# Performance work log

Hardware: AMD Instinct MI355X
Metric: run time of the kernel (lower is better)

## Reference

```python
import jax, jax.numpy as jnp
import numpy as np
import math

B = 2048
NOSC = 64            # oscillators per modality
M = 3                # modalities (audio, text, vision) in sorted order
BDIM = 256           # binding_dim
DT = 0.01
NSTEPS = 10
DIMS = [512, 768, 1024]  # audio, text, vision
TWO_PI = 2.0 * math.pi


def setup_inputs() -> dict:
    key = jax.random.key(0)
    ks = iter(jax.random.split(key, 40))
    d = {}
    names = ['a', 't', 'v']
    for name, dim, x_key in zip(names, DIMS, ['x_audio', 'x_text', 'x_vision']):
        d[x_key] = jax.random.normal(next(ks), (B, dim), dtype=jnp.float32)
        s = 1.0 / math.sqrt(dim)
        d[f'Wf_{name}'] = jax.random.uniform(next(ks), (BDIM, dim), jnp.float32, -s, s)
        d[f'bf_{name}'] = jax.random.uniform(next(ks), (BDIM,), jnp.float32, -s, s)
        d[f'Wp_{name}'] = jax.random.uniform(next(ks), (NOSC, dim), jnp.float32, -s, s)
        d[f'bp_{name}'] = jax.random.uniform(next(ks), (NOSC,), jnp.float32, -s, s)
    # omegas: randn*0.1 + 1.0 + i*0.5 for i-th sorted modality
    for i, name in enumerate(names):
        d[f'omega_{name}'] = jax.random.normal(next(ks), (NOSC,), jnp.float32) * 0.1 + 1.0 + i * 0.5
    N = M * NOSC
    d['inter_coupling'] = jax.random.normal(next(ks), (N, N), jnp.float32) * 0.1
    s = 1.0 / math.sqrt(BDIM * M)
    d['W_fusion'] = jax.random.uniform(next(ks), (BDIM, BDIM * M), jnp.float32, -s, s)
    d['b_fusion'] = jax.random.uniform(next(ks), (BDIM,), jnp.float32, -s, s)
    return d


def reference(x_audio, x_text, x_vision,
              Wf_a, bf_a, Wp_a, bp_a,
              Wf_t, bf_t, Wp_t, bp_t,
              Wf_v, bf_v, Wp_v, bp_v,
              omega_a, omega_t, omega_v,
              inter_coupling, W_fusion, b_fusion):
    def enc(x, Wf, bf, Wp, bp):
        encoded = x @ Wf.T + bf                       # (B, BDIM)
        phases = (x @ Wp.T + bp) % TWO_PI             # (B, NOSC)
        return encoded, phases

    e_a, p_a = enc(x_audio, Wf_a, bf_a, Wp_a, bp_a)
    e_t, p_t = enc(x_text, Wf_t, bf_t, Wp_t, bp_t)
    e_v, p_v = enc(x_vision, Wf_v, bf_v, Wp_v, bp_v)

    phases = jnp.concatenate([p_a, p_t, p_v], axis=-1)        # (B, N)
    omega = jnp.concatenate([omega_a, omega_t, omega_v])      # (N,)
    K = (inter_coupling + inter_coupling.T) * 0.5             # (N, N)
    N = phases.shape[-1]

    def step(ph, _):
        diff = ph[:, :, None] - ph[:, None, :]                # (B, N, N)
        forces = jnp.einsum('ij,bij->bi', K, jnp.sin(diff)) / N
        ph = (ph + DT * (omega[None, :] + forces)) % TWO_PI
        return ph, None

    phases, _ = jax.lax.scan(step, phases, None, length=NSTEPS)

    pm = [phases[:, i * NOSC:(i + 1) * NOSC] for i in range(M)]  # per-modality

    # PLV between banks a,b: |mean_{i,j} exp(i(a_i - b_j))| = R_a * R_b where
    # R = |mean_k exp(i phi_k)| (resultant length), computed with real math.
    R = jnp.stack([jnp.sqrt(jnp.mean(jnp.cos(p), -1) ** 2 +
                            jnp.mean(jnp.sin(p), -1) ** 2) for p in pm])  # (M, B)
    bm = jnp.mean(R[:, None, :] * R[None, :, :], axis=-1)      # (M, M)
    binding_matrix = jnp.where(jnp.eye(M, dtype=bool), 1.0, bm)

    fused_parts = []
    for e, p in zip([e_a, e_t, e_v], pm):
        phase_mod = jnp.mean(jnp.cos(p), axis=-1, keepdims=True)  # (B, 1)
        fused_parts.append(e * (0.5 + 0.5 * phase_mod))
    fused = jnp.concatenate(fused_parts, axis=-1)              # (B, M*BDIM)
    bound = fused @ W_fusion.T + b_fusion                      # (B, BDIM)

    triu = jnp.triu(jnp.ones((M, M), dtype=bool), k=1)
    total = jnp.sum(jnp.where(triu, binding_matrix, 0.0)) / triu.sum()
    total_binding = jnp.full((bound.shape[0],), total)

    return bound, binding_matrix, phases, total_binding
```

## Files before the change

### kernel.cpp

```cpp
#include <hip/hip_runtime.h>
#include <math.h>

typedef short bf16x8 __attribute__((ext_vector_type(8)));
typedef short bf16x4 __attribute__((ext_vector_type(4)));
typedef float f32x4  __attribute__((ext_vector_type(4)));

#define INV_2PI  0.15915494309189535f
#define TWO_PI_F 6.283185307179586f
#define FSCALE   8.2893199e-06f

static __device__ inline short f2bf(float f) {
    union { float f; unsigned u; } v; v.f = f;
    unsigned r = (v.u + 0x7FFFu + ((v.u >> 16) & 1u)) >> 16;
    return (short)r;
}
static __device__ inline float bf2f(short h) {
    union { unsigned u; float f; } v; v.u = ((unsigned)(unsigned short)h) << 16;
    return v.f;
}

__global__ __launch_bounds__(256) void front_kernel(
    const float* __restrict__ xa, const float* __restrict__ xt, const float* __restrict__ xv,
    const float* __restrict__ Wpa, const float* __restrict__ Wpt, const float* __restrict__ Wpv,
    const float* __restrict__ Wfa, const float* __restrict__ Wft, const float* __restrict__ Wfv,
    const float* __restrict__ Wfu,
    const float* __restrict__ IC,
    const float* __restrict__ oa, const float* __restrict__ ot, const float* __restrict__ ov,
    const float* __restrict__ bpa, const float* __restrict__ bpt, const float* __restrict__ bpv,
    float* __restrict__ partial, short* __restrict__ XB, short* __restrict__ WB,
    short* __restrict__ Kp,
    float* __restrict__ om_eff, float* __restrict__ bp_all, float* __restrict__ bacc)
{
    __shared__ alignas(16) float As[16][72];
    __shared__ alignas(16) float Bs[16][72];
    int b = blockIdx.x;
    int t = threadIdx.x;

    if (b < 576) {
        int slot = b % 18, rb = b / 18;
        int z = slot < 4 ? 0 : (slot < 10 ? 1 : 2);
        int chunk = slot - (z == 0 ? 0 : (z == 1 ? 4 : 10));
        const float* A = z == 0 ? xa : (z == 1 ? xt : xv);
        const float* W = z == 0 ? Wpa : (z == 1 ? Wpt : Wpv);
        short* XBz = XB + (z == 0 ? 0 : (z == 1 ? 1048576 : 2621440));
        int K = z == 0 ? 512 : (z == 1 ? 768 : 1024);
        int kb = chunk * 128;
        int m0 = rb * 64;

        int tx = t & 15, ty = t >> 4;
        int row = t >> 2, c4 = t & 3;

        float acc[4][4] = {};
        float4 ar = *(const float4*)&A[(size_t)(m0 + row) * K + kb + c4 * 4];
        float4 br = *(const float4*)&W[(size_t)row * K + kb + c4 * 4];

        for (int k0 = 0; k0 < 128; k0 += 16) {
            if (k0) __syncthreads();
            As[c4 * 4 + 0][row] = ar.x;
            As[c4 * 4 + 1][row] = ar.y;
            As[c4 * 4 + 2][row] = ar.z;
            As[c4 * 4 + 3][row] = ar.w;
            Bs[c4 * 4 + 0][row] = br.x;
            Bs[c4 * 4 + 1][row] = br.y;
            Bs[c4 * 4 + 2][row] = br.z;
            Bs[c4 * 4 + 3][row] = br.w;
            {
                bf16x4 h; h[0] = f2bf(ar.x); h[1] = f2bf(ar.y);
                h[2] = f2bf(ar.z); h[3] = f2bf(ar.w);
                *(bf16x4*)&XBz[(size_t)(m0 + row) * K + kb + k0 + c4 * 4] = h;
            }
            __syncthreads();
            if (k0 + 16 < 128) {
                ar = *(const float4*)&A[(size_t)(m0 + row) * K + kb + k0 + 16 + c4 * 4];
                br = *(const float4*)&W[(size_t)row * K + kb + k0 + 16 + c4 * 4];
            }
#pragma unroll
            for (int kk = 0; kk < 16; ++kk) {
                float4 aq = *(const float4*)&As[kk][ty * 4];
                float4 bq = *(const float4*)&Bs[kk][tx * 4];
                float av[4] = {aq.x, aq.y, aq.z, aq.w};
                float bv[4] = {bq.x, bq.y, bq.z, bq.w};
#pragma unroll
                for (int i = 0; i < 4; ++i)
#pragma unroll
                    for (int j = 0; j < 4; ++j)
                        acc[i][j] += av[i] * bv[j];
            }
        }

#pragma unroll
        for (int i = 0; i < 4; ++i) {
            int row_l = ty * 4 + i;
            int qb = rb * 4 + (row_l >> 4), rloc = row_l & 15;
            float4 v = make_float4(acc[i][0], acc[i][1], acc[i][2], acc[i][3]);
            *(float4*)&partial[((size_t)(qb * 18 + slot)) * 1024 + rloc * 64 + tx * 4] = v;
        }
    } else if (b < 600) {
        for (int u = (b - 576) * 256 + t; u < 196608; u += 24 * 256) {
            const float4* sp;
            if (u < 32768)       sp = (const float4*)Wfa + u;
            else if (u < 81920)  sp = (const float4*)Wft + (u - 32768);
            else if (u < 147456) sp = (const float4*)Wfv + (u - 81920);
            else                 sp = (const float4*)Wfu + (u - 147456);
            float4 v = *sp;
            bf16x4 h; h[0] = f2bf(v.x); h[1] = f2bf(v.y); h[2] = f2bf(v.z); h[3] = f2bf(v.w);
            *(bf16x4*)(WB + (size_t)u * 4) = h;
        }
    } else if (b < 632) {
        for (int idx = (b - 600) * 256 + t; idx < 36864; idx += 32 * 256) {
            int k = idx / 192, n = idx - k * 192;
            float v = 0.5f * (IC[k * 192 + n] + IC[n * 192 + k]);
            int nt = n >> 4, kc = k >> 5;
            int lane = ((k >> 3) & 3) * 16 + (n & 15);
            int j = k & 7;
            Kp[((nt * 6 + kc) * 64 + lane) * 8 + j] = f2bf(v);
        }
    } else {
        if (t < 192) {
            float w = t < 64 ? oa[t] : (t < 128 ? ot[t - 64] : ov[t - 128]);
            om_eff[t] = w * (0.01f * INV_2PI);
            float bb = t < 64 ? bpa[t] : (t < 128 ? bpt[t - 64] : bpv[t - 128]);
            bp_all[t] = bb;
        }
        if (t < 4) bacc[t] = 0.f;
    }
}

__global__ __launch_bounds__(256) void mid_kernel(
    const short* __restrict__ XB, const short* __restrict__ WB,
    const float* __restrict__ ba, const float* __restrict__ bt, const float* __restrict__ bv,
    const float* __restrict__ partial, const float* __restrict__ bp_all,
    const short* __restrict__ Kp, const float* __restrict__ om_eff,
    short* __restrict__ e_bf16,
    float* __restrict__ phases_out, float* __restrict__ pm, float* __restrict__ bacc)
{
    __shared__ alignas(16) char smem[27840];
    int b = blockIdx.x;
    int t = threadIdx.x;
    int lane = t & 63, w = t >> 6;
    int q = lane >> 4, col = lane & 15;

    if (b >= 128) {
        int bb = b - 128;
        int z = bb / 128, r = bb % 128;
        int m0 = (r >> 2) * 64, n0 = (r & 3) * 64;
        const short* A    = XB + (z == 0 ? 0 : (z == 1 ? 1048576 : 2621440));
        const short* W    = WB + (z == 0 ? 0 : (z == 1 ? 131072 : 327680));
        const float* bias = z == 0 ? ba : (z == 1 ? bt : bv);
        int K             = z == 0 ? 512 : (z == 1 ? 768 : 1024);

        short* As = (short*)smem;
        short* Bs = (short*)smem + 64 * 72;

        int srow = t >> 3, sc8 = t & 7;

        f32x4 acc[4];
#pragma unroll
        for (int f = 0; f < 4; ++f)
#pragma unroll
            for (int rr = 0; rr < 4; ++rr) acc[f][rr] = 0.f;

        bf16x8 av[2], bv8[2];
#pragma unroll
        for (int p = 0; p < 2; ++p) {
            av[p]  = *(const bf16x8*)&A[(size_t)(m0 + srow + 32 * p) * K + sc8 * 8];
            bv8[p] = *(const bf16x8*)&W[(size_t)(n0 + srow + 32 * p) * K + sc8 * 8];
        }

        for (int kb = 0; kb < K; kb += 64) {
            if (kb) __syncthreads();
#pragma unroll
            for (int p = 0; p < 2; ++p) {
                *(bf16x8*)&As[(srow + 32 * p) * 72 + sc8 * 8] = av[p];
                *(bf16x8*)&Bs[(srow + 32 * p) * 72 + sc8 * 8] = bv8[p];
            }
            __syncthreads();
            if (kb + 64 < K) {
#pragma unroll
                for (int p = 0; p < 2; ++p) {
                    av[p]  = *(const bf16x8*)&A[(size_t)(m0 + srow + 32 * p) * K + kb + 64 + sc8 * 8];
                    bv8[p] = *(const bf16x8*)&W[(size_t)(n0 + srow + 32 * p) * K + kb + 64 + sc8 * 8];
                }
            }

            bf16x8 bfr[2];
#pragma unroll
            for (int kc = 0; kc < 2; ++kc)
                bfr[kc] = *(const bf16x8*)&Bs[(w * 16 + col) * 72 + kc * 32 + q * 8];
#pragma unroll
            for (int f = 0; f < 4; ++f)
#pragma unroll
                for (int kc = 0; kc < 2; ++kc) {
                    bf16x8 af = *(const bf16x8*)&As[(f * 16 + col) * 72 + kc * 32 + q * 8];
                    acc[f] = __builtin_amdgcn_mfma_f32_16x16x32_bf16(af, bfr[kc], acc[f], 0, 0, 0);
                }
        }

        int n = n0 + w * 16 + col;
        float bn = bias[n];
#pragma unroll
        for (int f = 0; f < 4; ++f)
#pragma unroll
            for (int rr = 0; rr < 4; ++rr) {
                int m = m0 + f * 16 + q * 4 + rr;
                e_bf16[(size_t)m * 768 + z * 256 + n] = f2bf(acc[f][rr] + bn);
            }
    } else {
        short (*cs)[2][16][216] = (short (*)[2][16][216])smem;
        float (*Rl)[3] = (float (*)[3])(smem + 27648);
        float* ph0 = (float*)smem;

        int m0 = b * 16;

        bf16x8 kb[3][6];
#pragma unroll
        for (int ntl = 0; ntl < 3; ++ntl)
#pragma unroll
            for (int kc = 0; kc < 6; ++kc) {
                int nt = w * 3 + ntl;
                kb[ntl][kc] = *(const bf16x8*)&Kp[((nt * 6 + kc) * 64 + lane) * 8];
            }

        {
            const float* Pb = partial + (size_t)b * 18 * 1024;
            f32x4 s0, s1, s2;
#pragma unroll
            for (int j = 0; j < 4; ++j) { s0[j] = 0.f; s1[j] = 0.f; s2[j] = 0.f; }
#pragma unroll
            for (int s = 0; s < 18; ++s) {
                f32x4 v = *(const f32x4*)&Pb[s * 1024 + t * 4];
                if (s < 4)       s0 += v;
                else if (s < 10) s1 += v;
                else             s2 += v;
            }
            int row = t >> 4, c4 = t & 15;
            *(f32x4*)&ph0[row * 196 +   0 + c4 * 4] = s0;
            *(f32x4*)&ph0[row * 196 +  64 + c4 * 4] = s1;
            *(f32x4*)&ph0[row * 196 + 128 + c4 * 4] = s2;
        }
        __syncthreads();

        float ph[3][4], om[3], c[3][4], s[3][4];
#pragma unroll
        for (int ntl = 0; ntl < 3; ++ntl) {
            int i = (w * 3 + ntl) * 16 + col;
            om[ntl] = om_eff[i];
#pragma unroll
            for (int r = 0; r < 4; ++r) {
                float raw = bp_all[i] + ph0[(q * 4 + r) * 196 + i];
                raw *= INV_2PI;
                ph[ntl][r] = raw - floorf(raw);
            }
        }
        __syncthreads();

        for (int step = 0; step < 10; ++step) {
            int p = step & 1;
#pragma unroll
            for (int ntl = 0; ntl < 3; ++ntl) {
                int i = (w * 3 + ntl) * 16 + col;
#pragma unroll
                for (int r = 0; r < 4; ++r) {
                    c[ntl][r] = __builtin_amdgcn_cosf(ph[ntl][r]);
                    s[ntl][r] = __builtin_amdgcn_sinf(ph[ntl][r]);
                    cs[p][0][q * 4 + r][i] = f2bf(c[ntl][r]);
                    cs[p][1][q * 4 + r][i] = f2bf(s[ntl][r]);
                }
            }
            __syncthreads();

            f32x4 aC[3], aS[3];
#pragma unroll
            for (int ntl = 0; ntl < 3; ++ntl)
#pragma unroll
                for (int r = 0; r < 4; ++r) { aC[ntl][r] = 0.f; aS[ntl][r] = 0.f; }

#pragma unroll
            for (int kc = 0; kc < 6; ++kc) {
                bf16x8 ac  = *(const bf16x8*)&cs[p][0][col][kc * 32 + q * 8];
                bf16x8 as_ = *(const bf16x8*)&cs[p][1][col][kc * 32 + q * 8];
#pragma unroll
                for (int ntl = 0; ntl < 3; ++ntl) {
                    aC[ntl] = __builtin_amdgcn_mfma_f32_16x16x32_bf16(ac,  kb[ntl][kc], aC[ntl], 0, 0, 0);
                    aS[ntl] = __builtin_amdgcn_mfma_f32_16x16x32_bf16(as_, kb[ntl][kc], aS[ntl], 0, 0, 0);
                }
            }

#pragma unroll
            for (int ntl = 0; ntl < 3; ++ntl)
#pragma unroll
                for (int r = 0; r < 4; ++r) {
                    float f = (s[ntl][r] * aC[ntl][r] - c[ntl][r] * aS[ntl][r]) * FSCALE;
                    float pn = ph[ntl][r] + om[ntl] + f;
                    ph[ntl][r] = pn - floorf(pn);
                }
        }

#pragma unroll
        for (int ntl = 0; ntl < 3; ++ntl) {
            int i = (w * 3 + ntl) * 16 + col;
#pragma unroll
            for (int r = 0; r < 4; ++r) {
                float cp = __builtin_amdgcn_cosf(ph[ntl][r]);
                float sp = __builtin_amdgcn_sinf(ph[ntl][r]);
                cs[0][0][q * 4 + r][i] = f2bf(cp);
                cs[0][1][q * 4 + r][i] = f2bf(sp);
                phases_out[(size_t)(m0 + q * 4 + r) * 192 + i] = ph[ntl][r] * TWO_PI_F;
            }
        }
        __syncthreads();

        if (t < 48) {
            int r = t & 15, mod = t >> 4;
            float sc = 0.f, ss = 0.f;
#pragma unroll
            for (int g = 0; g < 8; ++g) {
                bf16x8 vc = *(const bf16x8*)&cs[0][0][r][mod * 64 + g * 8];
                bf16x8 vs = *(const bf16x8*)&cs[0][1][r][mod * 64 + g * 8];
#pragma unroll
                for (int j = 0; j < 8; ++j) { sc += bf2f(vc[j]); ss += bf2f(vs[j]); }
            }
            sc *= (1.f / 64.f); ss *= (1.f / 64.f);
            pm[(size_t)(m0 + r) * 3 + mod] = 0.5f + 0.5f * sc;
            Rl[r][mod] = sqrtf(sc * sc + ss * ss);
        }
        __syncthreads();
        if (t < 3) {
            int a = (t == 2) ? 1 : 0;
            int bb = (t == 0) ? 1 : 2;
            float accp = 0.f;
            for (int r = 0; r < 16; ++r) accp += Rl[r][a] * Rl[r][bb];
            atomicAdd(&bacc[t], accp);
        }
    }
}

__global__ __launch_bounds__(256) void back_kernel(
    const short* __restrict__ e_bf16, const short* __restrict__ WB,
    const float* __restrict__ bias, const float* __restrict__ pm,
    const float* __restrict__ bacc,
    float* __restrict__ out_bound, float* __restrict__ out_bm, float* __restrict__ out_total)
{
    const short* Wfb = WB + 589824;
    __shared__ alignas(16) short As2[16 * 776];

    int m0 = blockIdx.x * 16, n0 = blockIdx.y * 128;
    int t = threadIdx.x;
    int lane = t & 63, w = t >> 6;
    int q = lane >> 4, col = lane & 15;

#pragma unroll
    for (int i = 0; i < 6; ++i) {
        int g = t + 256 * i;
        int rw = g / 96, cg = g - rw * 96;
        float sc = pm[(size_t)(m0 + rw) * 3 + (cg >> 5)];
        bf16x8 v = *(const bf16x8*)&e_bf16[(size_t)(m0 + rw) * 768 + cg * 8];
        bf16x8 h;
#pragma unroll
        for (int j = 0; j < 8; ++j) h[j] = f2bf(bf2f(v[j]) * sc);
        *(bf16x8*)&As2[rw * 776 + cg * 8] = h;
    }
    __syncthreads();

    f32x4 facc[2];
#pragma unroll
    for (int j = 0; j < 2; ++j)
#pragma unroll
        for (int rr = 0; rr < 4; ++rr) facc[j][rr] = 0.f;

    int n_[2];
#pragma unroll
    for (int j = 0; j < 2; ++j) n_[j] = n0 + (w * 2 + j) * 16 + col;

    bf16x8 bcur[2], bnxt[2];
#pragma unroll
    for (int j = 0; j < 2; ++j)
        bcur[j] = *(const bf16x8*)&Wfb[(size_t)n_[j] * 768 + q * 8];

    for (int k0 = 0; k0 < 768; k0 += 32) {
        if (k0 + 32 < 768) {
#pragma unroll
            for (int j = 0; j < 2; ++j)
                bnxt[j] = *(const bf16x8*)&Wfb[(size_t)n_[j] * 768 + k0 + 32 + q * 8];
        }
        bf16x8 af = *(const bf16x8*)&As2[col * 776 + k0 + q * 8];
#pragma unroll
        for (int j = 0; j < 2; ++j)
            facc[j] = __builtin_amdgcn_mfma_f32_16x16x32_bf16(af, bcur[j], facc[j], 0, 0, 0);
#pragma unroll
        for (int j = 0; j < 2; ++j) bcur[j] = bnxt[j];
    }

#pragma unroll
    for (int j = 0; j < 2; ++j) {
        float bn = bias[n_[j]];
#pragma unroll
        for (int rr = 0; rr < 4; ++rr) {
            int m = m0 + q * 4 + rr;
            out_bound[(size_t)m * 256 + n_[j]] = facc[j][rr] + bn;
        }
    }

    if (blockIdx.x == 0 && blockIdx.y == 0) {
        float p01 = bacc[0] * (1.f / 2048.f);
        float p02 = bacc[1] * (1.f / 2048.f);
        float p12 = bacc[2] * (1.f / 2048.f);
        float total = (p01 + p02 + p12) * (1.f / 3.f);
        if (t == 0) {
            out_bm[0] = 1.f; out_bm[1] = p01; out_bm[2] = p02;
            out_bm[3] = p01; out_bm[4] = 1.f; out_bm[5] = p12;
            out_bm[6] = p02; out_bm[7] = p12; out_bm[8] = 1.f;
        }
        for (int i = t; i < 2048; i += 256) out_total[i] = total;
    }
}

extern "C" void kernel_launch(void* const* d_in, const int* in_sizes, int n_in,
                              void* d_out, int out_size, void* d_ws, size_t ws_size,
                              hipStream_t stream)
{
    const float* x_a  = (const float*)d_in[0];
    const float* Wf_a = (const float*)d_in[1];
    const float* bf_a = (const float*)d_in[2];
    const float* Wp_a = (const float*)d_in[3];
    const float* bp_a = (const float*)d_in[4];
    const float* x_t  = (const float*)d_in[5];
    const float* Wf_t = (const float*)d_in[6];
    const float* bf_t = (const float*)d_in[7];
    const float* Wp_t = (const float*)d_in[8];
    const float* bp_t = (const float*)d_in[9];
    const float* x_v  = (const float*)d_in[10];
    const float* Wf_v = (const float*)d_in[11];
    const float* bf_v = (const float*)d_in[12];
    const float* Wp_v = (const float*)d_in[13];
    const float* bp_v = (const float*)d_in[14];
    const float* om_a = (const float*)d_in[15];
    const float* om_t = (const float*)d_in[16];
    const float* om_v = (const float*)d_in[17];
    const float* IC   = (const float*)d_in[18];
    const float* Wfu  = (const float*)d_in[19];
    const float* bfu  = (const float*)d_in[20];

    float* ws      = (float*)d_ws;
    float* omw     = ws;
    float* bpw     = ws + 256;
    float* pmv     = ws + 512;
    float* baccw   = ws + 6656;
    float* partial = ws + 6720;
    short* e_bf    = (short*)(ws + 2366016);
    short* XB      = (short*)(ws + 3152448);
    short* Kpck    = (short*)(ws + 5511744);
    short* WB      = (short*)(ws + 5530176);

    float* out        = (float*)d_out;
    float* out_bound  = out;
    float* out_bm     = out + 524288;
    float* out_phases = out + 524297;
    float* out_total  = out + 917513;

    front_kernel<<<633, 256, 0, stream>>>(
        x_a, x_t, x_v, Wp_a, Wp_t, Wp_v, Wf_a, Wf_t, Wf_v, Wfu,
        IC, om_a, om_t, om_v, bp_a, bp_t, bp_v,
        partial, XB, WB, Kpck, omw, bpw, baccw);

    mid_kernel<<<512, 256, 0, stream>>>(
        XB, WB, bf_a, bf_t, bf_v,
        partial, bpw, Kpck, omw,
        e_bf, out_phases, pmv, baccw);

    dim3 gF(128, 2);
    back_kernel<<<gF, 256, 0, stream>>>(e_bf, WB, bfu, pmv, baccw,
                                        out_bound, out_bm, out_total);
}
```

Baseline: 142.3 us.

## Fuse back GEMM into mid kernel with counter-based spin waits

Merges the fusion GEMM (formerly back_kernel) into mid_kernel as extra blocks that spin on global atomic counters until the Kuramoto block and the encoder GEMM row-tiles they depend on have finished. The x-to-bf16 conversion moves out of the phase-GEMM loop into dedicated conversion blocks, and the binding accumulation now writes per-block partials that the last finishing block reduces. This removes one kernel launch and its drain/fill gap, and lets the back GEMM overlap the tail of the mid work. It relies on dependency blocks being scheduled before waiting blocks to avoid deadlock, and adds spin and fence overhead.

```diff
diff --git a/kernel.cpp b/kernel.cpp
--- a/kernel.cpp
+++ b/kernel.cpp
@@ -29,7 +29,7 @@
     const float* __restrict__ bpa, const float* __restrict__ bpt, const float* __restrict__ bpv,
     float* __restrict__ partial, short* __restrict__ XB, short* __restrict__ WB,
     short* __restrict__ Kp,
-    float* __restrict__ om_eff, float* __restrict__ bp_all, float* __restrict__ bacc)
+    float* __restrict__ om_eff, float* __restrict__ bp_all, unsigned* __restrict__ ctr)
 {
     __shared__ alignas(16) float As[16][72];
     __shared__ alignas(16) float Bs[16][72];
@@ -42,7 +42,6 @@
         int chunk = slot - (z == 0 ? 0 : (z == 1 ? 4 : 10));
         const float* A = z == 0 ? xa : (z == 1 ? xt : xv);
         const float* W = z == 0 ? Wpa : (z == 1 ? Wpt : Wpv);
-        short* XBz = XB + (z == 0 ? 0 : (z == 1 ? 1048576 : 2621440));
         int K = z == 0 ? 512 : (z == 1 ? 768 : 1024);
         int kb = chunk * 128;
         int m0 = rb * 64;
@@ -64,11 +63,6 @@
             Bs[c4 * 4 + 1][row] = br.y;
             Bs[c4 * 4 + 2][row] = br.z;
             Bs[c4 * 4 + 3][row] = br.w;
-            {
-                bf16x4 h; h[0] = f2bf(ar.x); h[1] = f2bf(ar.y);
-                h[2] = f2bf(ar.z); h[3] = f2bf(ar.w);
-                *(bf16x4*)&XBz[(size_t)(m0 + row) * K + kb + k0 + c4 * 4] = h;
-            }
             __syncthreads();
             if (k0 + 16 < 128) {
                 ar = *(const float4*)&A[(size_t)(m0 + row) * K + kb + k0 + 16 + c4 * 4];
@@ -95,19 +89,30 @@
             float4 v = make_float4(acc[i][0], acc[i][1], acc[i][2], acc[i][3]);
             *(float4*)&partial[((size_t)(qb * 18 + slot)) * 1024 + rloc * 64 + tx * 4] = v;
         }
-    } else if (b < 600) {
-        for (int u = (b - 576) * 256 + t; u < 196608; u += 24 * 256) {
-            const float4* sp;
-            if (u < 32768)       sp = (const float4*)Wfa + u;
-            else if (u < 81920)  sp = (const float4*)Wft + (u - 32768);
-            else if (u < 147456) sp = (const float4*)Wfv + (u - 81920);
-            else                 sp = (const float4*)Wfu + (u - 147456);
-            float4 v = *sp;
-            bf16x4 h; h[0] = f2bf(v.x); h[1] = f2bf(v.y); h[2] = f2bf(v.z); h[3] = f2bf(v.w);
-            *(bf16x4*)(WB + (size_t)u * 4) = h;
-        }
-    } else if (b < 632) {
-        for (int idx = (b - 600) * 256 + t; idx < 36864; idx += 32 * 256) {
+    } else if (b < 672) {
+        for (int u = (b - 576) * 256 + t; u < 1376256; u += 96 * 256) {
+            if (u < 1179648) {
+                const float4* sp;
+                if (u < 262144)      sp = (const float4*)xa + u;
+                else if (u < 655360) sp = (const float4*)xt + (u - 262144);
+                else                 sp = (const float4*)xv + (u - 655360);
+                float4 v = *sp;
+                bf16x4 h; h[0] = f2bf(v.x); h[1] = f2bf(v.y); h[2] = f2bf(v.z); h[3] = f2bf(v.w);
+                *(bf16x4*)&XB[(size_t)u * 4] = h;
+            } else {
+                int uw = u - 1179648;
+                const float4* sp;
+                if (uw < 32768)       sp = (const float4*)Wfa + uw;
+                else if (uw < 81920)  sp = (const float4*)Wft + (uw - 32768);
+                else if (uw < 147456) sp = (const float4*)Wfv + (uw - 81920);
+                else                  sp = (const float4*)Wfu + (uw - 147456);
+                float4 v = *sp;
+                bf16x4 h; h[0] = f2bf(v.x); h[1] = f2bf(v.y); h[2] = f2bf(v.z); h[3] = f2bf(v.w);
+                *(bf16x4*)(WB + (size_t)uw * 4) = h;
+            }
+        }
+    } else if (b < 704) {
+        for (int idx = (b - 672) * 256 + t; idx < 36864; idx += 32 * 256) {
             int k = idx / 192, n = idx - k * 192;
             float v = 0.5f * (IC[k * 192 + n] + IC[n * 192 + k]);
             int nt = n >> 4, kc = k >> 5;
@@ -122,7 +127,7 @@
             float bb = t < 64 ? bpa[t] : (t < 128 ? bpt[t - 64] : bpv[t - 128]);
             bp_all[t] = bb;
         }
-        if (t < 4) bacc[t] = 0.f;
+        if (t < 160) ctr[t] = 0;
     }
 }
 
@@ -132,15 +137,149 @@
     const float* __restrict__ partial, const float* __restrict__ bp_all,
     const short* __restrict__ Kp, const float* __restrict__ om_eff,
     short* __restrict__ e_bf16,
-    float* __restrict__ phases_out, float* __restrict__ pm, float* __restrict__ bacc)
+    float* __restrict__ phases_out, float* __restrict__ pm,
+    float* __restrict__ bacc_part, unsigned* __restrict__ ctr,
+    const float* __restrict__ bfu,
+    float* __restrict__ out_bound, float* __restrict__ out_bm, float* __restrict__ out_total)
 {
-    __shared__ alignas(16) char smem[27840];
+    __shared__ alignas(16) char smem[27904];
     int b = blockIdx.x;
     int t = threadIdx.x;
     int lane = t & 63, w = t >> 6;
     int q = lane >> 4, col = lane & 15;
 
-    if (b >= 128) {
+    if (b < 128) {
+        short (*cs)[2][16][216] = (short (*)[2][16][216])smem;
+        float (*Rl)[3] = (float (*)[3])(smem + 27648);
+        float* ph0 = (float*)smem;
+
+        int g = b;
+        int m0 = g * 16;
+
+        bf16x8 kb[3][6];
+#pragma unroll
+        for (int ntl = 0; ntl < 3; ++ntl)
+#pragma unroll
+            for (int kc = 0; kc < 6; ++kc) {
+                int nt = w * 3 + ntl;
+                kb[ntl][kc] = *(const bf16x8*)&Kp[((nt * 6 + kc) * 64 + lane) * 8];
+            }
+
+        {
+            const float* Pb = partial + (size_t)g * 18 * 1024;
+            f32x4 s0, s1, s2;
+#pragma unroll
+            for (int j = 0; j < 4; ++j) { s0[j] = 0.f; s1[j] = 0.f; s2[j] = 0.f; }
+#pragma unroll
+            for (int s = 0; s < 18; ++s) {
+                f32x4 v = *(const f32x4*)&Pb[s * 1024 + t * 4];
+                if (s < 4)       s0 += v;
+                else if (s < 10) s1 += v;
+                else             s2 += v;
+            }
+            int row = t >> 4, c4 = t & 15;
+            *(f32x4*)&ph0[row * 196 +   0 + c4 * 4] = s0;
+            *(f32x4*)&ph0[row * 196 +  64 + c4 * 4] = s1;
+            *(f32x4*)&ph0[row * 196 + 128 + c4 * 4] = s2;
+        }
+        __syncthreads();
+
+        float ph[3][4], om[3], c[3][4], s[3][4];
+#pragma unroll
+        for (int ntl = 0; ntl < 3; ++ntl) {
+            int i = (w * 3 + ntl) * 16 + col;
+            om[ntl] = om_eff[i];
+#pragma unroll
+            for (int r = 0; r < 4; ++r) {
+                float raw = bp_all[i] + ph0[(q * 4 + r) * 196 + i];
+                raw *= INV_2PI;
+                ph[ntl][r] = raw - floorf(raw);
+            }
+        }
+        __syncthreads();
+
+        for (int step = 0; step < 10; ++step) {
+            int p = step & 1;
+#pragma unroll
+            for (int ntl = 0; ntl < 3; ++ntl) {
+                int i = (w * 3 + ntl) * 16 + col;
+#pragma unroll
+                for (int r = 0; r < 4; ++r) {
+                    c[ntl][r] = __builtin_amdgcn_cosf(ph[ntl][r]);
+                    s[ntl][r] = __builtin_amdgcn_sinf(ph[ntl][r]);
+                    cs[p][0][q * 4 + r][i] = f2bf(c[ntl][r]);
+                    cs[p][1][q * 4 + r][i] = f2bf(s[ntl][r]);
+                }
+            }
+            __syncthreads();
+
+            f32x4 aC[3], aS[3];
+#pragma unroll
+            for (int ntl = 0; ntl < 3; ++ntl)
+#pragma unroll
+                for (int r = 0; r < 4; ++r) { aC[ntl][r] = 0.f; aS[ntl][r] = 0.f; }
+
+#pragma unroll
+            for (int kc = 0; kc < 6; ++kc) {
+                bf16x8 ac  = *(const bf16x8*)&cs[p][0][col][kc * 32 + q * 8];
+                bf16x8 as_ = *(const bf16x8*)&cs[p][1][col][kc * 32 + q * 8];
+#pragma unroll
+                for (int ntl = 0; ntl < 3; ++ntl) {
+                    aC[ntl] = __builtin_amdgcn_mfma_f32_16x16x32_bf16(ac,  kb[ntl][kc], aC[ntl], 0, 0, 0);
+                    aS[ntl] = __builtin_amdgcn_mfma_f32_16x16x32_bf16(as_, kb[ntl][kc], aS[ntl], 0, 0, 0);
+                }
+            }
+
+#pragma unroll
+            for (int ntl = 0; ntl < 3; ++ntl)
+#pragma unroll
+                for (int r = 0; r < 4; ++r) {
+                    float f = (s[ntl][r] * aC[ntl][r] - c[ntl][r] * aS[ntl][r]) * FSCALE;
+                    float pn = ph[ntl][r] + om[ntl] + f;
+                    ph[ntl][r] = pn - floorf(pn);
+                }
+        }
+
+#pragma unroll
+        for (int ntl = 0; ntl < 3; ++ntl) {
+            int i = (w * 3 + ntl) * 16 + col;
+#pragma unroll
+            for (int r = 0; r < 4; ++r) {
+                float cp = __builtin_amdgcn_cosf(ph[ntl][r]);
+                float sp = __builtin_amdgcn_sinf(ph[ntl][r]);
+                cs[0][0][q * 4 + r][i] = f2bf(cp);
+                cs[0][1][q * 4 + r][i] = f2bf(sp);
+                phases_out[(size_t)(m0 + q * 4 + r) * 192 + i] = ph[ntl][r] * TWO_PI_F;
+            }
+        }
+        __syncthreads();
+
+        if (t < 48) {
+            int r = t & 15, mod = t >> 4;
+            float sc = 0.f, ss = 0.f;
+#pragma unroll
+            for (int gg = 0; gg < 8; ++gg) {
+                bf16x8 vc = *(const bf16x8*)&cs[0][0][r][mod * 64 + gg * 8];
+                bf16x8 vs = *(const bf16x8*)&cs[0][1][r][mod * 64 + gg * 8];
+#pragma unroll
+                for (int j = 0; j < 8; ++j) { sc += bf2f(vc[j]); ss += bf2f(vs[j]); }
+            }
+            sc *= (1.f / 64.f); ss *= (1.f / 64.f);
+            pm[(size_t)(m0 + r) * 3 + mod] = 0.5f + 0.5f * sc;
+            Rl[r][mod] = sqrtf(sc * sc + ss * ss);
+        }
+        __syncthreads();
+        if (t < 3) {
+            int a = (t == 2) ? 1 : 0;
+            int bb2 = (t == 0) ? 1 : 2;
+            float accp = 0.f;
+            for (int r = 0; r < 16; ++r) accp += Rl[r][a] * Rl[r][bb2];
+            bacc_part[g * 4 + t] = accp;
+        }
+        __threadfence();
+        __syncthreads();
+        if (t == 0) atomicAdd(&ctr[16 + g], 1u);
+    } else if (b < 512) {
         int bb = b - 128;
         int z = bb / 128, r = bb % 128;
         int m0 = (r >> 2) * 64, n0 = (r & 3) * 64;
@@ -205,213 +344,103 @@
                 int m = m0 + f * 16 + q * 4 + rr;
                 e_bf16[(size_t)m * 768 + z * 256 + n] = f2bf(acc[f][rr] + bn);
             }
+        __threadfence();
+        __syncthreads();
+        if (t == 0) atomicAdd(&ctr[r >> 2], 1u);
     } else {
-        short (*cs)[2][16][216] = (short (*)[2][16][216])smem;
-        float (*Rl)[3] = (float (*)[3])(smem + 27648);
-        float* ph0 = (float*)smem;
-
-        int m0 = b * 16;
-
-        bf16x8 kb[3][6];
-#pragma unroll
-        for (int ntl = 0; ntl < 3; ++ntl)
-#pragma unroll
-            for (int kc = 0; kc < 6; ++kc) {
-                int nt = w * 3 + ntl;
-                kb[ntl][kc] = *(const bf16x8*)&Kp[((nt * 6 + kc) * 64 + lane) * 8];
-            }
-
-        {
-            const float* Pb = partial + (size_t)b * 18 * 1024;
-            f32x4 s0, s1, s2;
-#pragma unroll
-            for (int j = 0; j < 4; ++j) { s0[j] = 0.f; s1[j] = 0.f; s2[j] = 0.f; }
-#pragma unroll
-            for (int s = 0; s < 18; ++s) {
-                f32x4 v = *(const f32x4*)&Pb[s * 1024 + t * 4];
-                if (s < 4)       s0 += v;
-                else if (s < 10) s1 += v;
-                else             s2 += v;
-            }
-            int row = t >> 4, c4 = t & 15;
-            *(f32x4*)&ph0[row * 196 +   0 + c4 * 4] = s0;
-            *(f32x4*)&ph0[row * 196 +  64 + c4 * 4] = s1;
-            *(f32x4*)&ph0[row * 196 + 128 + c4 * 4] = s2;
-        }
-        __syncthreads();
-
-        float ph[3][4], om[3], c[3][4], s[3][4];
-#pragma unroll
-        for (int ntl = 0; ntl < 3; ++ntl) {
-            int i = (w * 3 + ntl) * 16 + col;
-            om[ntl] = om_eff[i];
-#pragma unroll
-            for (int r = 0; r < 4; ++r) {
-                float raw = bp_all[i] + ph0[(q * 4 + r) * 196 + i];
-                raw *= INV_2PI;
-                ph[ntl][r] = raw - floorf(raw);
-            }
-        }
-        __syncthreads();
-
-        for (int step = 0; step < 10; ++step) {
-            int p = step & 1;
-#pragma unroll
-            for (int ntl = 0; ntl < 3; ++ntl) {
-                int i = (w * 3 + ntl) * 16 + col;
-#pragma unroll
-                for (int r = 0; r < 4; ++r) {
-                    c[ntl][r] = __builtin_amdgcn_cosf(ph[ntl][r]);
-                    s[ntl][r] = __builtin_amdgcn_sinf(ph[ntl][r]);
-                    cs[p][0][q * 4 + r][i] = f2bf(c[ntl][r]);
-                    cs[p][1][q * 4 + r][i] = f2bf(s[ntl][r]);
-                }
+        short* As2 = (short*)smem;
+        float* fsum = (float*)(smem + 24832);
+        unsigned* sflag = (unsigned*)(smem + 27840);
+
+        int fb = b - 512;
+        int g = fb >> 1;
+        int m0 = g * 16, n0 = (fb & 1) * 128;
+        const short* Wfb = WB + 589824;
+
+        if (t == 0) {
+            while (atomicAdd(&ctr[16 + g], 0u) < 1u) __builtin_amdgcn_s_sleep(2);
+            while (atomicAdd(&ctr[g >> 2], 0u) < 12u) __builtin_amdgcn_s_sleep(2);
+        }
+        __syncthreads();
+        __threadfence();
+
+#pragma unroll
+        for (int i = 0; i < 6; ++i) {
+            int gg = t + 256 * i;
+            int rw = gg / 96, cg = gg - rw * 96;
+            float sc = pm[(size_t)(m0 + rw) * 3 + (cg >> 5)];
+            bf16x8 v = *(const bf16x8*)&e_bf16[(size_t)(m0 + rw) * 768 + cg * 8];
+            bf16x8 h;
+#pragma unroll
+            for (int j = 0; j < 8; ++j) h[j] = f2bf(bf2f(v[j]) * sc);
+            *(bf16x8*)&As2[rw * 776 + cg * 8] = h;
+        }
+        __syncthreads();
+
+        f32x4 facc[2];
+#pragma unroll
+        for (int j = 0; j < 2; ++j)
+#pragma unroll
+            for (int rr = 0; rr < 4; ++rr) facc[j][rr] = 0.f;
+
+        int n_[2];
+#pragma unroll
+        for (int j = 0; j < 2; ++j) n_[j] = n0 + (w * 2 + j) * 16 + col;
+
+        bf16x8 bcur[2], bnxt[2];
+#pragma unroll
+        for (int j = 0; j < 2; ++j)
+            bcur[j] = *(const bf16x8*)&Wfb[(size_t)n_[j] * 768 + q * 8];
+
+        for (int k0 = 0; k0 < 768; k0 += 32) {
+            if (k0 + 32 < 768) {
+#pragma unroll
+                for (int j = 0; j < 2; ++j)
+                    bnxt[j] = *(const bf16x8*)&Wfb[(size_t)n_[j] * 768 + k0 + 32 + q * 8];
+            }
+            bf16x8 af = *(const bf16x8*)&As2[col * 776 + k0 + q * 8];
+#pragma unroll
+            for (int j = 0; j < 2; ++j)
+                facc[j] = __builtin_amdgcn_mfma_f32_16x16x32_bf16(af, bcur[j], facc[j], 0, 0, 0);
+#pragma unroll
+            for (int j = 0; j < 2; ++j) bcur[j] = bnxt[j];
+        }
+
+#pragma unroll
+        for (int j = 0; j < 2; ++j) {
+            float bn = bfu[n_[j]];
+#pragma unroll
+            for (int rr = 0; rr < 4; ++rr) {
+                int m = m0 + q * 4 + rr;
+                out_bound[(size_t)m * 256 + n_[j]] = facc[j][rr] + bn;
+            }
+        }
+
+        if (t == 0) {
+            __threadfence();
+            unsigned r = atomicAdd(&ctr[144], 1u);
+            *sflag = (r == 255u) ? 1u : 0u;
+        }
+        __syncthreads();
+        if (*sflag) {
+            __threadfence();
+            if (t < 3) {
+                float s = 0.f;
+                for (int gg = 0; gg < 128; ++gg) s += bacc_part[gg * 4 + t];
+                fsum[t] = s;
             }
             __syncthreads();
-
-            f32x4 aC[3], aS[3];
-#pragma unroll
-            for (int ntl = 0; ntl < 3; ++ntl)
-#pragma unroll
-                for (int r = 0; r < 4; ++r) { aC[ntl][r] = 0.f; aS[ntl][r] = 0.f; }
-
-#pragma unroll
-            for (int kc = 0; kc < 6; ++kc) {
-                bf16x8 ac  = *(const bf16x8*)&cs[p][0][col][kc * 32 + q * 8];
-                bf16x8 as_ = *(const bf16x8*)&cs[p][1][col][kc * 32 + q * 8];
-#pragma unroll
-                for (int ntl = 0; ntl < 3; ++ntl) {
-                    aC[ntl] = __builtin_amdgcn_mfma_f32_16x16x32_bf16(ac,  kb[ntl][kc], aC[ntl], 0, 0, 0);
-                    aS[ntl] = __builtin_amdgcn_mfma_f32_16x16x32_bf16(as_, kb[ntl][kc], aS[ntl], 0, 0, 0);
-                }
-            }
-
-#pragma unroll
-            for (int ntl = 0; ntl < 3; ++ntl)
-#pragma unroll
-                for (int r = 0; r < 4; ++r) {
-                    float f = (s[ntl][r] * aC[ntl][r] - c[ntl][r] * aS[ntl][r]) * FSCALE;
-                    float pn = ph[ntl][r] + om[ntl] + f;
-                    ph[ntl][r] = pn - floorf(pn);
-                }
-        }
-
-#pragma unroll
-        for (int ntl = 0; ntl < 3; ++ntl) {
-            int i = (w * 3 + ntl) * 16 + col;
-#pragma unroll
-            for (int r = 0; r < 4; ++r) {
-                float cp = __builtin_amdgcn_cosf(ph[ntl][r]);
-                float sp = __builtin_amdgcn_sinf(ph[ntl][r]);
-                cs[0][0][q * 4 + r][i] = f2bf(cp);
-                cs[0][1][q * 4 + r][i] = f2bf(sp);
-                phases_out[(size_t)(m0 + q * 4 + r) * 192 + i] = ph[ntl][r] * TWO_PI_F;
-            }
-        }
-        __syncthreads();
-
-        if (t < 48) {
-            int r = t & 15, mod = t >> 4;
-            float sc = 0.f, ss = 0.f;
-#pragma unroll
-            for (int g = 0; g < 8; ++g) {
-                bf16x8 vc = *(const bf16x8*)&cs[0][0][r][mod * 64 + g * 8];
-                bf16x8 vs = *(const bf16x8*)&cs[0][1][r][mod * 64 + g * 8];
-#pragma unroll
-                for (int j = 0; j < 8; ++j) { sc += bf2f(vc[j]); ss += bf2f(vs[j]); }
-            }
-            sc *= (1.f / 64.f); ss *= (1.f / 64.f);
-            pm[(size_t)(m0 + r) * 3 + mod] = 0.5f + 0.5f * sc;
-            Rl[r][mod] = sqrtf(sc * sc + ss * ss);
-        }
-        __syncthreads();
-        if (t < 3) {
-            int a = (t == 2) ? 1 : 0;
-            int bb = (t == 0) ? 1 : 2;
-            float accp = 0.f;
-            for (int r = 0; r < 16; ++r) accp += Rl[r][a] * Rl[r][bb];
-            atomicAdd(&bacc[t], accp);
-        }
-    }
-}
-
-__global__ __launch_bounds__(256) void back_kernel(
-    const short* __restrict__ e_bf16, const short* __restrict__ WB,
-    const float* __restrict__ bias, const float* __restrict__ pm,
-    const float* __restrict__ bacc,
-    float* __restrict__ out_bound, float* __restrict__ out_bm, float* __restrict__ out_total)
-{
-    const short* Wfb = WB + 589824;
-    __shared__ alignas(16) short As2[16 * 776];
-
-    int m0 = blockIdx.x * 16, n0 = blockIdx.y * 128;
-    int t = threadIdx.x;
-    int lane = t & 63, w = t >> 6;
-    int q = lane >> 4, col = lane & 15;
-
-#pragma unroll
-    for (int i = 0; i < 6; ++i) {
-        int g = t + 256 * i;
-        int rw = g / 96, cg = g - rw * 96;
-        float sc = pm[(size_t)(m0 + rw) * 3 + (cg >> 5)];
-        bf16x8 v = *(const bf16x8*)&e_bf16[(size_t)(m0 + rw) * 768 + cg * 8];
-        bf16x8 h;
-#pragma unroll
-        for (int j = 0; j < 8; ++j) h[j] = f2bf(bf2f(v[j]) * sc);
-        *(bf16x8*)&As2[rw * 776 + cg * 8] = h;
-    }
-    __syncthreads();
-
-    f32x4 facc[2];
-#pragma unroll
-    for (int j = 0; j < 2; ++j)
-#pragma unroll
-        for (int rr = 0; rr < 4; ++rr) facc[j][rr] = 0.f;
-
-    int n_[2];
-#pragma unroll
-    for (int j = 0; j < 2; ++j) n_[j] = n0 + (w * 2 + j) * 16 + col;
-
-    bf16x8 bcur[2], bnxt[2];
-#pragma unroll
-    for (int j = 0; j < 2; ++j)
-        bcur[j] = *(const bf16x8*)&Wfb[(size_t)n_[j] * 768 + q * 8];
-
-    for (int k0 = 0; k0 < 768; k0 += 32) {
-        if (k0 + 32 < 768) {
-#pragma unroll
-            for (int j = 0; j < 2; ++j)
-                bnxt[j] = *(const bf16x8*)&Wfb[(size_t)n_[j] * 768 + k0 + 32 + q * 8];
-        }
-        bf16x8 af = *(const bf16x8*)&As2[col * 776 + k0 + q * 8];
-#pragma unroll
-        for (int j = 0; j < 2; ++j)
-            facc[j] = __builtin_amdgcn_mfma_f32_16x16x32_bf16(af, bcur[j], facc[j], 0, 0, 0);
-#pragma unroll
-        for (int j = 0; j < 2; ++j) bcur[j] = bnxt[j];
-    }
-
-#pragma unroll
-    for (int j = 0; j < 2; ++j) {
-        float bn = bias[n_[j]];
-#pragma unroll
-        for (int rr = 0; rr < 4; ++rr) {
-            int m = m0 + q * 4 + rr;
-            out_bound[(size_t)m * 256 + n_[j]] = facc[j][rr] + bn;
-        }
-    }
-
-    if (blockIdx.x == 0 && blockIdx.y == 0) {
-        float p01 = bacc[0] * (1.f / 2048.f);
-        float p02 = bacc[1] * (1.f / 2048.f);
-        float p12 = bacc[2] * (1.f / 2048.f);
-        float total = (p01 + p02 + p12) * (1.f / 3.f);
-        if (t == 0) {
-            out_bm[0] = 1.f; out_bm[1] = p01; out_bm[2] = p02;
-            out_bm[3] = p01; out_bm[4] = 1.f; out_bm[5] = p12;
-            out_bm[6] = p02; out_bm[7] = p12; out_bm[8] = 1.f;
-        }
-        for (int i = t; i < 2048; i += 256) out_total[i] = total;
+            float p01 = fsum[0] * (1.f / 2048.f);
+            float p02 = fsum[1] * (1.f / 2048.f);
+            float p12 = fsum[2] * (1.f / 2048.f);
+            float total = (p01 + p02 + p12) * (1.f / 3.f);
+            if (t == 0) {
+                out_bm[0] = 1.f; out_bm[1] = p01; out_bm[2] = p02;
+                out_bm[3] = p01; out_bm[4] = 1.f; out_bm[5] = p12;
+                out_bm[6] = p02; out_bm[7] = p12; out_bm[8] = 1.f;
+            }
+            for (int i = t; i < 2048; i += 256) out_total[i] = total;
+        }
     }
 }
 
@@ -441,16 +470,17 @@
     const float* Wfu  = (const float*)d_in[19];
     const float* bfu  = (const float*)d_in[20];
 
-    float* ws      = (float*)d_ws;
-    float* omw     = ws;
-    float* bpw     = ws + 256;
-    float* pmv     = ws + 512;
-    float* baccw   = ws + 6656;
-    float* partial = ws + 6720;
-    short* e_bf    = (short*)(ws + 2366016);
-    short* XB      = (short*)(ws + 3152448);
-    short* Kpck    = (short*)(ws + 5511744);
-    short* WB      = (short*)(ws + 5530176);
+    float* ws        = (float*)d_ws;
+    float* omw       = ws;
+    float* bpw       = ws + 256;
+    float* pmv       = ws + 512;
+    unsigned* ctrw   = (unsigned*)(ws + 6656);
+    float* baccp     = ws + 6816;
+    float* partial   = ws + 7328;
+    short* e_bf      = (short*)(ws + 2366624);
+    short* XB        = (short*)(ws + 3153056);
+    short* Kpck      = (short*)(ws + 5512352);
+    short* WB        = (short*)(ws + 5530784);
 
     float* out        = (float*)d_out;
     float* out_bound  = out;
@@ -458,17 +488,14 @@
     float* out_phases = out + 524297;
     float* out_total  = out + 917513;
 
-    front_kernel<<<633, 256, 0, stream>>>(
+    front_kernel<<<705, 256, 0, stream>>>(
         x_a, x_t, x_v, Wp_a, Wp_t, Wp_v, Wf_a, Wf_t, Wf_v, Wfu,
         IC, om_a, om_t, om_v, bp_a, bp_t, bp_v,
-        partial, XB, WB, Kpck, omw, bpw, baccw);
-
-    mid_kernel<<<512, 256, 0, stream>>>(
+        partial, XB, WB, Kpck, omw, bpw, ctrw);
+
+    mid_kernel<<<768, 256, 0, stream>>>(
         XB, WB, bf_a, bf_t, bf_v,
         partial, bpw, Kpck, omw,
-        e_bf, out_phases, pmv, baccw);
-
-    dim3 gF(128, 2);
-    back_kernel<<<gF, 256, 0, stream>>>(e_bf, WB, bfu, pmv, baccw,
-                                        out_bound, out_bm, out_total);
+        e_bf, out_phases, pmv, baccp, ctrw,
+        bfu, out_bound, out_bm, out_total);
 }
```

Result: slower. 248.9 us (+74.9%).

## Stage full 128-wide K chunk in shared memory before phase GEMM

Applied to the files above, without the earlier changes.

The phase-projection GEMM branch now loads the whole 128-element K chunk of A and W into registers up front, writes it to enlarged shared tiles (128x72 each), and syncs once. The previous version streamed 16-wide slices with two barriers per step. This removes the repeated barriers and issues all global loads at once for more memory-level parallelism. The cost is about 72 KB of static LDS and more registers in the front kernel, which may cut occupancy for every branch of that kernel. The other edits only rename variables.

```diff
diff --git a/kernel.cpp b/kernel.cpp
--- a/kernel.cpp
+++ b/kernel.cpp
@@ -31,8 +31,8 @@
     short* __restrict__ Kp,
     float* __restrict__ om_eff, float* __restrict__ bp_all, float* __restrict__ bacc)
 {
-    __shared__ alignas(16) float As[16][72];
-    __shared__ alignas(16) float Bs[16][72];
+    __shared__ alignas(16) float As[128][72];
+    __shared__ alignas(16) float Bs[128][72];
     int b = blockIdx.x;
     int t = threadIdx.x;
 
@@ -48,44 +48,44 @@
         int m0 = rb * 64;
 
         int tx = t & 15, ty = t >> 4;
-        int row = t >> 2, c4 = t & 3;
+        int r  = t >> 2, c4 = t & 3;
+
+        float4 af4[8], bf4[8];
+#pragma unroll
+        for (int i = 0; i < 8; ++i) {
+            int c = c4 + 4 * i;
+            af4[i] = *(const float4*)&A[(size_t)(m0 + r) * K + kb + c * 4];
+            bf4[i] = *(const float4*)&W[(size_t)r * K + kb + c * 4];
+        }
+#pragma unroll
+        for (int i = 0; i < 8; ++i) {
+            int c = c4 + 4 * i;
+            As[c * 4 + 0][r] = af4[i].x;
+            As[c * 4 + 1][r] = af4[i].y;
+            As[c * 4 + 2][r] = af4[i].z;
+            As[c * 4 + 3][r] = af4[i].w;
+            Bs[c * 4 + 0][r] = bf4[i].x;
+            Bs[c * 4 + 1][r] = bf4[i].y;
+            Bs[c * 4 + 2][r] = bf4[i].z;
+            Bs[c * 4 + 3][r] = bf4[i].w;
+            bf16x4 h; h[0] = f2bf(af4[i].x); h[1] = f2bf(af4[i].y);
+            h[2] = f2bf(af4[i].z); h[3] = f2bf(af4[i].w);
+            *(bf16x4*)&XBz[(size_t)(m0 + r) * K + kb + c * 4] = h;
+        }
+        __syncthreads();
 
         float acc[4][4] = {};
-        float4 ar = *(const float4*)&A[(size_t)(m0 + row) * K + kb + c4 * 4];
-        float4 br = *(const float4*)&W[(size_t)row * K + kb + c4 * 4];
-
-        for (int k0 = 0; k0 < 128; k0 += 16) {
-            if (k0) __syncthreads();
-            As[c4 * 4 + 0][row] = ar.x;
-            As[c4 * 4 + 1][row] = ar.y;
-            As[c4 * 4 + 2][row] = ar.z;
-            As[c4 * 4 + 3][row] = ar.w;
-            Bs[c4 * 4 + 0][row] = br.x;
-            Bs[c4 * 4 + 1][row] = br.y;
-            Bs[c4 * 4 + 2][row] = br.z;
-            Bs[c4 * 4 + 3][row] = br.w;
-            {
-                bf16x4 h; h[0] = f2bf(ar.x); h[1] = f2bf(ar.y);
-                h[2] = f2bf(ar.z); h[3] = f2bf(ar.w);
-                *(bf16x4*)&XBz[(size_t)(m0 + row) * K + kb + k0 + c4 * 4] = h;
-            }
-            __syncthreads();
-            if (k0 + 16 < 128) {
-                ar = *(const float4*)&A[(size_t)(m0 + row) * K + kb + k0 + 16 + c4 * 4];
-                br = *(const float4*)&W[(size_t)row * K + kb + k0 + 16 + c4 * 4];
-            }
-#pragma unroll
-            for (int kk = 0; kk < 16; ++kk) {
-                float4 aq = *(const float4*)&As[kk][ty * 4];
-                float4 bq = *(const float4*)&Bs[kk][tx * 4];
-                float av[4] = {aq.x, aq.y, aq.z, aq.w};
-                float bv[4] = {bq.x, bq.y, bq.z, bq.w};
-#pragma unroll
-                for (int i = 0; i < 4; ++i)
-#pragma unroll
-                    for (int j = 0; j < 4; ++j)
-                        acc[i][j] += av[i] * bv[j];
-            }
+#pragma unroll 4
+        for (int k = 0; k < 128; ++k) {
+            float4 aq = *(const float4*)&As[k][ty * 4];
+            float4 bq = *(const float4*)&Bs[k][tx * 4];
+            float av[4] = {aq.x, aq.y, aq.z, aq.w};
+            float bv[4] = {bq.x, bq.y, bq.z, bq.w};
+#pragma unroll
+            for (int i = 0; i < 4; ++i)
+#pragma unroll
+                for (int j = 0; j < 4; ++j)
+                    acc[i][j] += av[i] * bv[j];
         }
 
 #pragma unroll
@@ -210,7 +210,8 @@
         float (*Rl)[3] = (float (*)[3])(smem + 27648);
         float* ph0 = (float*)smem;
 
-        int m0 = b * 16;
+        int g = b;
+        int m0 = g * 16;
 
         bf16x8 kb[3][6];
 #pragma unroll
@@ -222,7 +223,7 @@
             }
 
         {
-            const float* Pb = partial + (size_t)b * 18 * 1024;
+            const float* Pb = partial + (size_t)g * 18 * 1024;
             f32x4 s0, s1, s2;
 #pragma unroll
             for (int j = 0; j < 4; ++j) { s0[j] = 0.f; s1[j] = 0.f; s2[j] = 0.f; }
@@ -314,9 +315,9 @@
             int r = t & 15, mod = t >> 4;
             float sc = 0.f, ss = 0.f;
 #pragma unroll
-            for (int g = 0; g < 8; ++g) {
-                bf16x8 vc = *(const bf16x8*)&cs[0][0][r][mod * 64 + g * 8];
-                bf16x8 vs = *(const bf16x8*)&cs[0][1][r][mod * 64 + g * 8];
+            for (int gg = 0; gg < 8; ++gg) {
+                bf16x8 vc = *(const bf16x8*)&cs[0][0][r][mod * 64 + gg * 8];
+                bf16x8 vs = *(const bf16x8*)&cs[0][1][r][mod * 64 + gg * 8];
 #pragma unroll
                 for (int j = 0; j < 8; ++j) { sc += bf2f(vc[j]); ss += bf2f(vs[j]); }
             }
```

Measured after the change: 152.4 us. 7.1% more time.
